# Optimization experiments

Hardware: AMD Instinct MI355X
Metric: run time of the kernel (lower is better)

The kernel has to match this reference:

```python
import jax, jax.numpy as jnp
import numpy as np

N, E = 50000, 1600000
D_IN, D_OUT = 256, 64
ALPHA = 0.2        # LeakyReLU slope used on attention logits (self.leakyrelu)
BT_SLOPE = 0.01    # F.leaky_relu default slope inside relu_bt


def _xavier_normal(key, shape, gain):
    fan_in, fan_out = shape[0], shape[1]
    std = gain * np.sqrt(2.0 / (fan_in + fan_out))
    return jax.random.normal(key, shape, dtype=jnp.float32) * std


def relu_bt(x):
    # -threshold(-leaky_relu(x), -t, -t) == min(leaky_relu(x), t), t = ||x||_inf (detached)
    t = jax.lax.stop_gradient(jnp.max(jnp.abs(x)))
    y = jnp.where(x >= 0, x, BT_SLOPE * x)
    return jnp.minimum(y, t)


def setup_inputs() -> dict:
    key = jax.random.key(0)
    k0, k1, k2, k3, k4, k5 = jax.random.split(key, 6)
    inp = jax.random.normal(k0, (N, D_IN), dtype=jnp.float32)
    edge = jax.random.randint(k1, (2, E), 0, N, dtype=jnp.int64)
    W_high = _xavier_normal(k2, (D_IN, D_OUT), 1.414)
    W_low = _xavier_normal(k3, (D_IN, D_OUT), 1.414)
    a_high = _xavier_normal(k4, (1, D_OUT), 1.414)
    a_low = _xavier_normal(k5, (1, D_OUT), 1.414)
    return {"input": inp, "edge": edge, "W_high": W_high, "W_low": W_low,
            "a_high": a_high, "a_low": a_low}


def reference(input, edge, W_high, W_low, a_high, a_low):
    n = input.shape[0]
    src, dst = edge[0], edge[1]

    h_high = relu_bt(input @ W_high)  # [N, D_OUT]
    h_low = relu_bt(input @ W_low)    # [N, D_OUT]

    # a @ (h[src] -/+ h[dst])^T == (a.h)[src] -/+ (a.h)[dst]: compute per-node scalar
    # projections first, then gather scalars per edge (avoids [E, D_OUT] edge features).
    s_high = h_high @ a_high[0]       # [N]
    s_low = h_low @ a_low[0]          # [N]

    def lrelu(x):
        return jnp.where(x >= 0, x, ALPHA * x)

    edge_e_high = jnp.exp(-lrelu(s_high[src] - s_high[dst]))  # [E]
    edge_e_low = jnp.exp(-lrelu(s_low[src] + s_low[dst]))     # [E]
    # dropout p=0.0 -> identity

    # sparse A @ ones -> per-row sum of attention weights
    rowsum_high = jax.ops.segment_sum(edge_e_high, src, num_segments=n)[:, None]
    rowsum_low = jax.ops.segment_sum(edge_e_low, src, num_segments=n)[:, None]

    # sparse A @ h -> weighted aggregation of neighbor features
    hp_high = jax.ops.segment_sum(edge_e_high[:, None] * h_high[dst], src, num_segments=n)
    hp_low = jax.ops.segment_sum(edge_e_low[:, None] * h_low[dst], src, num_segments=n)

    hp_high = hp_high / (rowsum_high + 1e-16)
    hp_low = hp_low / (rowsum_low + 1e-16)

    # concat=True branch
    return relu_bt(jnp.concatenate([hp_high, hp_low], axis=1))  # [N, 2*D_OUT]
```

## Files before the change

### kernel.cpp

```cpp
#include <hip/hip_runtime.h>
#include <hip/hip_bf16.h>
#include <cstdint>

#define NN    50000
#define NE    1600000
#define DIN   256
#define DOUT  64
#define CAPS  96
#define CAPD  95

#define BKT   196
#define BCAP  10240
#define EPB   4096
#define EPT   16
#define NBIN  391
#define MTB   64
#define NGEMM 782

typedef __attribute__((ext_vector_type(8))) short frag8;
typedef __attribute__((ext_vector_type(4))) float fragc;

union PK { __hip_bfloat162 b2; uint32_t u; };
union CH { frag8 v; uint32_t u[4]; };

__device__ __forceinline__ float leaky01(float x) { return x >= 0.f ? x : 0.01f * x; }

__device__ __forceinline__ uint32_t pk2(float lo, float hi) {
  PK p; p.b2 = __float22bfloat162_rn(make_float2(lo, hi)); return p.u;
}

__device__ __forceinline__ int   bcast_i(int v, int lane) {
  return __builtin_amdgcn_readlane(v, lane);
}
__device__ __forceinline__ float bcast_f(float v, int lane) {
  return __int_as_float(__builtin_amdgcn_readlane(__float_as_int(v), lane));
}

__device__ __forceinline__ float bfH(uint32_t u) { return __uint_as_float(u << 16); }
__device__ __forceinline__ float bfL(uint32_t u) { return __uint_as_float(u & 0xffff0000u); }

__global__ __launch_bounds__(256) void prep_kernel(
    const float* __restrict__ Wh, const float* __restrict__ Wl,
    __hip_bfloat16* __restrict__ Wt, int* __restrict__ cursor)
{
  if (blockIdx.x == 0 && threadIdx.x < BKT) cursor[threadIdx.x] = 0;
  int g = blockIdx.x * 256 + threadIdx.x;
  if (g < 2 * DOUT * DIN) {
    int m = g >> 14, rem = g & 16383;
    int n = rem >> 8, k = rem & 255;
    float v = (m ? Wl : Wh)[k * DOUT + n];
    Wt[g] = __float2bfloat16(v);
  }
}

__global__ __launch_bounds__(256) void fused_kernel(
    const float* __restrict__ inp, const __hip_bfloat16* __restrict__ Wt,
    const float* __restrict__ ah, const float* __restrict__ al,
    const int* __restrict__ edge, int* __restrict__ cursor,
    uint32_t* __restrict__ binned, uint32_t* __restrict__ HL,
    float2* __restrict__ ss)
{
  __shared__ __align__(16) char smem[32768];

  const int idx = blockIdx.x;
  const int t = threadIdx.x;

  if (idx < NBIN) {
    uint32_t* stage  = (uint32_t*)smem;
    int*      hist   = (int*)(smem + 16384);
    int*      cur    = (int*)(smem + 17168);
    int*      base_g = (int*)(smem + 17952);
    int*      scan_s = (int*)(smem + 18736);

    const int e0 = idx * EPB;
    uint32_t v[EPT];
#pragma unroll
    for (int i = 0; i < EPT; i++) {
      int e = e0 + i * 256 + t;
      if (e < NE) {
        uint32_t s = (uint32_t)edge[e];
        uint32_t d = (uint32_t)edge[NE + e];
        v[i] = (s << 16) | d;
      } else {
        v[i] = 0xFFFFFFFFu;
      }
    }
    for (int b = t; b < BKT; b += 256) { hist[b] = 0; cur[b] = 0; }
    __syncthreads();
#pragma unroll
    for (int i = 0; i < EPT; i++) {
      int b = v[i] >> 24;
      if (b < BKT) atomicAdd(&hist[b], 1);
    }
    __syncthreads();
    if (t == 0) {
      int acc = 0;
      for (int b = 0; b < BKT; b++) { scan_s[b] = acc; acc += hist[b]; }
      scan_s[BKT] = acc;
    }
    __syncthreads();
    for (int b = t; b < BKT; b += 256) {
      int h = hist[b];
      base_g[b] = h ? atomicAdd(&cursor[b], h) : 0;
    }
    __syncthreads();
#pragma unroll
    for (int i = 0; i < EPT; i++) {
      int b = v[i] >> 24;
      if (b < BKT) {
        int pos = atomicAdd(&cur[b], 1);
        stage[scan_s[b] + pos] = v[i];
      }
    }
    __syncthreads();
    const int total = scan_s[BKT];
    for (int i = t; i < total; i += 256) {
      int lo = 0, hi = BKT - 1;
      while (lo < hi) { int mid = (lo + hi + 1) >> 1; if (scan_s[mid] <= i) lo = mid; else hi = mid - 1; }
      int ofs = base_g[lo] + (i - scan_s[lo]);
      if (ofs < BCAP) binned[(size_t)lo * BCAP + ofs] = stage[i];
    }
    return;
  }

  frag8* asmem = (frag8*)smem;
  const int gid = idx - NBIN;
  const int n0 = gid * MTB;
  const int lane = t & 63;
  const int w = t >> 6;
  const int quad = lane >> 4, nn = lane & 15;

  const frag8* Wt8 = (const frag8*)Wt;
  const int bbase = ((w * 16 + nn) << 5) + quad;
  frag8 bH[8], bL[8];
#pragma unroll
  for (int q = 0; q < 8; q++) {
    bH[q] = Wt8[bbase + (q << 2)];
    bL[q] = Wt8[2048 + bbase + (q << 2)];
  }

  const float4* inp4 = (const float4*)inp;
#pragma unroll
  for (int i = 0; i < 8; i++) {
    int c = i * 256 + t;
    int r = c & 15;
    int cc = c >> 4;
    int qd = cc & 3;
    int wq = cc >> 2;
    int row = ((wq >> 3) << 4) + r;
    int k0 = ((wq & 7) << 5) + (qd << 3);
    int node = n0 + row;
    float4 a0 = make_float4(0.f, 0.f, 0.f, 0.f), a1 = a0;
    if (node < NN) {
      a0 = inp4[(size_t)node * 64 + (k0 >> 2)];
      a1 = inp4[(size_t)node * 64 + (k0 >> 2) + 1];
    }
    CH ch;
    ch.u[0] = pk2(a0.x, a0.y);
    ch.u[1] = pk2(a0.z, a0.w);
    ch.u[2] = pk2(a1.x, a1.y);
    ch.u[3] = pk2(a1.z, a1.w);
    asmem[c] = ch.v;
  }
  __syncthreads();

  fragc accH[4], accL[4];
#pragma unroll
  for (int m = 0; m < 4; m++) {
    accH[m] = (fragc){0.f, 0.f, 0.f, 0.f};
    accL[m] = (fragc){0.f, 0.f, 0.f, 0.f};
  }

#pragma unroll
  for (int q = 0; q < 8; q++) {
#pragma unroll
    for (int mt = 0; mt < 4; mt++) {
      frag8 af = asmem[(mt << 9) + (q << 6) + lane];
      accH[mt] = __builtin_amdgcn_mfma_f32_16x16x32_bf16(af, bH[q], accH[mt], 0, 0, 0);
      accL[mt] = __builtin_amdgcn_mfma_f32_16x16x32_bf16(af, bL[q], accL[mt], 0, 0, 0);
    }
  }
  __syncthreads();

  float* sred = (float*)smem;
  const float ahv = ah[w * 16 + nn];
  const float alv = al[w * 16 + nn];
#pragma unroll
  for (int mt = 0; mt < 4; mt++) {
#pragma unroll
    for (int r = 0; r < 4; r++) {
      int rowb = (mt << 4) + (quad << 2) + r;
      int node = n0 + rowb;
      float hH = leaky01(accH[mt][r]);
      float hL = leaky01(accL[mt][r]);
      if (node < NN) HL[(size_t)node * DOUT + w * 16 + nn] = pk2(hH, hL);
      float pH = hH * ahv, pL = hL * alv;
#pragma unroll
      for (int off = 1; off < 16; off <<= 1) {
        pH += __shfl_xor(pH, off);
        pL += __shfl_xor(pL, off);
      }
      if (nn == 0) {
        sred[rowb * 8 + w]     = pH;
        sred[rowb * 8 + 4 + w] = pL;
      }
    }
  }
  __syncthreads();
  if (t < 64) {
    int node = n0 + t;
    if (node < NN) {
      float sH = sred[t * 8 + 0] + sred[t * 8 + 1] + sred[t * 8 + 2] + sred[t * 8 + 3];
      float sL = sred[t * 8 + 4] + sred[t * 8 + 5] + sred[t * 8 + 6] + sred[t * 8 + 7];
      ss[node] = make_float2(sH, sL);
    }
  }
}

__global__ __launch_bounds__(1024) void csr_kernel(
    const uint32_t* __restrict__ binned, const int* __restrict__ cursor,
    int* __restrict__ col)
{
  __shared__ int cnt[256];
  const int b = blockIdx.x;
  const int t = threadIdx.x;
  if (t < 256) cnt[t] = 0;
  __syncthreads();
  int n = cursor[b]; if (n > BCAP) n = BCAP;
  const uint32_t* eb = binned + (size_t)b * BCAP;
  for (int i = t; i < n; i += 1024) {
    uint32_t v = eb[i];
    int src = v >> 16, dst = v & 0xffff;
    int pos = atomicAdd(&cnt[src & 255], 1);
    if (pos < CAPD) col[(size_t)src * CAPS + 1 + pos] = dst;
  }
  __syncthreads();
  if (t < 256) {
    int node = (b << 8) + t;
    if (node < NN) {
      int c = cnt[t]; if (c > CAPD) c = CAPD;
      col[(size_t)node * CAPS] = c;
    }
  }
}

__global__ __launch_bounds__(256) void agg_kernel(
    const uint32_t* __restrict__ HL, const float2* __restrict__ ss,
    const int* __restrict__ col, float* __restrict__ out)
{
  int wave = (blockIdx.x * blockDim.x + threadIdx.x) >> 6;
  int lane = threadIdx.x & 63;
  if (wave >= NN) return;
  const int n = wave;
  const int* cl = col + (size_t)n * CAPS;
  int d = cl[0]; if (d > CAPD) d = CAPD;

  const float2 sn = ss[n];

  float accH = 0.f, accL = 0.f, rsH = 0.f, rsL = 0.f;

  for (int base = 0; base < d; base += 64) {
    int m = d - base; if (m > 64) m = 64;
    int   dst_l = 0;
    float eh_l = 0.f, el_l = 0.f;
    if (lane < m) {
      dst_l = cl[1 + base + lane];
      float2 sd = ss[dst_l];
      float xh = sn.x - sd.x;
      xh = (xh >= 0.f) ? xh : 0.2f * xh;
      eh_l = __expf(-xh);
      float xl = sn.y + sd.y;
      xl = (xl >= 0.f) ? xl : 0.2f * xl;
      el_l = __expf(-xl);
    }
    int j = 0;
    for (; j + 8 <= m; j += 8) {
      uint32_t u[8]; float eh[8], el[8];
#pragma unroll
      for (int x = 0; x < 8; x++) {
        int dd = bcast_i(dst_l, j + x);
        u[x]  = HL[((uint32_t)dd << 6) + lane];
        eh[x] = bcast_f(eh_l, j + x);
        el[x] = bcast_f(el_l, j + x);
      }
#pragma unroll
      for (int x = 0; x < 8; x++) {
        accH += eh[x] * bfH(u[x]); accL += el[x] * bfL(u[x]);
        rsH += eh[x]; rsL += el[x];
      }
    }
    for (; j < m; j++) {
      int      dst = bcast_i(dst_l, j);
      float    eh  = bcast_f(eh_l, j);
      float    el  = bcast_f(el_l, j);
      uint32_t u   = HL[((uint32_t)dst << 6) + lane];
      accH += eh * bfH(u);
      accL += el * bfL(u);
      rsH += eh;
      rsL += el;
    }
  }

  float oh = accH / (rsH + 1e-16f);
  float ol = accL / (rsL + 1e-16f);
  out[(size_t)n * 128 + lane]      = leaky01(oh);
  out[(size_t)n * 128 + 64 + lane] = leaky01(ol);
}

extern "C" void kernel_launch(void* const* d_in, const int* in_sizes, int n_in,
                              void* d_out, int out_size, void* d_ws, size_t ws_size,
                              hipStream_t stream) {
  const float* inp  = (const float*)d_in[0];
  const int*   edge = (const int*)d_in[1];
  const float* Wh   = (const float*)d_in[2];
  const float* Wl   = (const float*)d_in[3];
  const float* ah   = (const float*)d_in[4];
  const float* al   = (const float*)d_in[5];
  float* out = (float*)d_out;

  char* ws = (char*)d_ws;
  uint32_t* HL     = (uint32_t*)(ws + 0);
  float2*   ss     = (float2*)  (ws + 12800000);
  int*      col    = (int*)     (ws + 13200000);
  uint32_t* binned = (uint32_t*)(ws + 32400000);
  int*      cursor = (int*)     (ws + 40428160);
  __hip_bfloat16* Wt = (__hip_bfloat16*)(ws + 13200000);

  prep_kernel<<<128, 256, 0, stream>>>(Wh, Wl, Wt, cursor);
  fused_kernel<<<NBIN + NGEMM, 256, 0, stream>>>(inp, Wt, ah, al, edge,
                                                 cursor, binned, HL, ss);
  csr_kernel<<<BKT, 1024, 0, stream>>>(binned, cursor, col);
  agg_kernel<<<NN / 4, 256, 0, stream>>>(HL, ss, col, out);
}
```

Before: 197.2 us.

## Parallelize bucket scan, split CSR build across blocks, pad aggregation loop

The serial single-thread bucket prefix scan in the binning phase becomes a wave-level shuffle scan over four 64-wide segments. The CSR build is split into four blocks per bucket, each handling a quarter of the source nodes. This raises block count but means each block reads the whole bucket. The aggregation inner loop is unrolled by 16 with zero-padded neighbors, and row sums come from a wave-wide xor reduction instead of per-edge accumulation. That removes the tail loop but adds wasted gathers of node 0 for padded lanes.

```diff
diff --git a/kernel.cpp b/kernel.cpp
--- a/kernel.cpp
+++ b/kernel.cpp
@@ -16,6 +16,7 @@
 #define NBIN  391
 #define MTB   64
 #define NGEMM 782
+#define CSPL  4
 
 typedef __attribute__((ext_vector_type(8))) short frag8;
 typedef __attribute__((ext_vector_type(4))) float fragc;
@@ -68,9 +69,9 @@
   if (idx < NBIN) {
     uint32_t* stage  = (uint32_t*)smem;
     int*      hist   = (int*)(smem + 16384);
-    int*      cur    = (int*)(smem + 17168);
-    int*      base_g = (int*)(smem + 17952);
-    int*      scan_s = (int*)(smem + 18736);
+    int*      cur    = (int*)(smem + 17408);
+    int*      base_g = (int*)(smem + 18192);
+    int*      scan_s = (int*)(smem + 18976);
 
     const int e0 = idx * EPB;
     uint32_t v[EPT];
@@ -85,7 +86,8 @@
         v[i] = 0xFFFFFFFFu;
       }
     }
-    for (int b = t; b < BKT; b += 256) { hist[b] = 0; cur[b] = 0; }
+    if (t < 256) hist[t] = 0;
+    for (int b = t; b < BKT; b += 256) cur[b] = 0;
     __syncthreads();
 #pragma unroll
     for (int i = 0; i < EPT; i++) {
@@ -93,10 +95,22 @@
       if (b < BKT) atomicAdd(&hist[b], 1);
     }
     __syncthreads();
-    if (t == 0) {
-      int acc = 0;
-      for (int b = 0; b < BKT; b++) { scan_s[b] = acc; acc += hist[b]; }
-      scan_s[BKT] = acc;
+    if (t < 64) {
+      int carry = 0;
+#pragma unroll
+      for (int seg = 0; seg < 4; seg++) {
+        int i = seg * 64 + t;
+        int h = hist[i];
+        int s = h;
+#pragma unroll
+        for (int off = 1; off < 64; off <<= 1) {
+          int o = __shfl_up(s, off);
+          if (t >= off) s += o;
+        }
+        int excl = carry + s - h;
+        if (i <= BKT) scan_s[i] = excl;
+        carry += bcast_i(s, 63);
+      }
     }
     __syncthreads();
     for (int b = t; b < BKT; b += 256) {
@@ -217,26 +231,30 @@
   }
 }
 
-__global__ __launch_bounds__(1024) void csr_kernel(
+__global__ __launch_bounds__(256) void csr_kernel(
     const uint32_t* __restrict__ binned, const int* __restrict__ cursor,
     int* __restrict__ col)
 {
-  __shared__ int cnt[256];
-  const int b = blockIdx.x;
+  __shared__ int cnt[64];
+  const int b    = blockIdx.x / CSPL;
+  const int part = blockIdx.x % CSPL;
   const int t = threadIdx.x;
-  if (t < 256) cnt[t] = 0;
+  if (t < 64) cnt[t] = 0;
   __syncthreads();
   int n = cursor[b]; if (n > BCAP) n = BCAP;
   const uint32_t* eb = binned + (size_t)b * BCAP;
-  for (int i = t; i < n; i += 1024) {
+  for (int i = t; i < n; i += 256) {
     uint32_t v = eb[i];
     int src = v >> 16, dst = v & 0xffff;
-    int pos = atomicAdd(&cnt[src & 255], 1);
-    if (pos < CAPD) col[(size_t)src * CAPS + 1 + pos] = dst;
-  }
-  __syncthreads();
-  if (t < 256) {
-    int node = (b << 8) + t;
+    int loc = src & 255;
+    if ((loc >> 6) == part) {
+      int pos = atomicAdd(&cnt[loc & 63], 1);
+      if (pos < CAPD) col[(size_t)src * CAPS + 1 + pos] = dst;
+    }
+  }
+  __syncthreads();
+  if (t < 64) {
+    int node = (b << 8) + (part << 6) + t;
     if (node < NN) {
       int c = cnt[t]; if (c > CAPD) c = CAPD;
       col[(size_t)node * CAPS] = c;
@@ -273,32 +291,29 @@
       xl = (xl >= 0.f) ? xl : 0.2f * xl;
       el_l = __expf(-xl);
     }
-    int j = 0;
-    for (; j + 8 <= m; j += 8) {
-      uint32_t u[8]; float eh[8], el[8];
-#pragma unroll
-      for (int x = 0; x < 8; x++) {
+    const int mm = (m + 15) & ~15;
+    for (int j = 0; j < mm; j += 16) {
+      uint32_t u[16]; float eh[16], el[16];
+#pragma unroll
+      for (int x = 0; x < 16; x++) {
         int dd = bcast_i(dst_l, j + x);
         u[x]  = HL[((uint32_t)dd << 6) + lane];
         eh[x] = bcast_f(eh_l, j + x);
         el[x] = bcast_f(el_l, j + x);
       }
 #pragma unroll
-      for (int x = 0; x < 8; x++) {
-        accH += eh[x] * bfH(u[x]); accL += el[x] * bfL(u[x]);
-        rsH += eh[x]; rsL += el[x];
-      }
-    }
-    for (; j < m; j++) {
-      int      dst = bcast_i(dst_l, j);
-      float    eh  = bcast_f(eh_l, j);
-      float    el  = bcast_f(el_l, j);
-      uint32_t u   = HL[((uint32_t)dst << 6) + lane];
-      accH += eh * bfH(u);
-      accL += el * bfL(u);
-      rsH += eh;
-      rsL += el;
-    }
+      for (int x = 0; x < 16; x++) {
+        accH += eh[x] * bfH(u[x]);
+        accL += el[x] * bfL(u[x]);
+      }
+    }
+    float rh = eh_l, rl = el_l;
+#pragma unroll
+    for (int off = 1; off < 64; off <<= 1) {
+      rh += __shfl_xor(rh, off);
+      rl += __shfl_xor(rl, off);
+    }
+    rsH += rh; rsL += rl;
   }
 
   float oh = accH / (rsH + 1e-16f);
@@ -329,6 +344,6 @@
   prep_kernel<<<128, 256, 0, stream>>>(Wh, Wl, Wt, cursor);
   fused_kernel<<<NBIN + NGEMM, 256, 0, stream>>>(inp, Wt, ah, al, edge,
                                                  cursor, binned, HL, ss);
-  csr_kernel<<<BKT, 1024, 0, stream>>>(binned, cursor, col);
+  csr_kernel<<<BKT * CSPL, 256, 0, stream>>>(binned, cursor, col);
   agg_kernel<<<NN / 4, 256, 0, stream>>>(HL, ss, col, out);
 }
```

Result: slower. 203.6 us (+3.2%).
